# Optimization experiments

Measured on AMD Instinct MI355X. Metric: run time of the kernel, lower is better.

## Reference

```python
import jax, jax.numpy as jnp
import numpy as np

NB_TASKS = 20
CLASSES_PER_TASK = 100  # uniform cfg.increments -> cache_repeat
TOPK = 2
TEMPERATURE = 5.0  # cfg.task_temperature


def setup_inputs() -> dict:
    key = jax.random.key(0)
    k1, k2, k3 = jax.random.split(key, 3)
    B = 8192
    N = NB_TASKS * CLASSES_PER_TASK
    return {
        "gol": jax.random.normal(k1, (B, NB_TASKS), dtype=jnp.float32),
        "gocls": jax.random.normal(k2, (B, N), dtype=jnp.float32),
        "do_logit": jax.random.normal(k3, (B, N), dtype=jnp.float32),
        "alpha": jnp.array([0.5], dtype=jnp.float32),
    }


def _masked(gol_use, do_logit):
    # mask_ = softmax(gol_use / T, dim=1).repeat_interleave(cache_repeat, dim=1)
    soft = jax.nn.softmax(gol_use / TEMPERATURE, axis=1)  # [B, T]
    # topk hard mask, scattered then repeated; hard*soft repeated == repeat(hard*soft)
    k = min(gol_use.shape[1], TOPK)
    _, tk = jax.lax.top_k(gol_use, k)  # [B, k] int indices
    B = gol_use.shape[0]
    hard = jnp.zeros_like(gol_use).at[jnp.arange(B)[:, None], tk].set(1.0)
    mask = jnp.repeat(hard * soft, CLASSES_PER_TASK, axis=1)  # [B, N]
    return do_logit * mask


def reference(gol, gocls, do_logit, alpha):
    B = gol.shape[0]
    # gocl = opt_by_task(gate_cls_logit, increments, 'amax'): per-task max over class logits
    gocl = gocls.reshape(B, NB_TASKS, CLASSES_PER_TASK).max(axis=-1)  # [B, T]
    logit_mcm = _masked(gol, do_logit)
    logit_gcl = _masked(gocl, do_logit)
    lamb = alpha  # broadcasts over [B, N]
    logit_mix = lamb * logit_mcm + (1.0 - lamb) * logit_gcl
    return logit_mix
```

## Files before the change

kernel.cpp:

```cpp
#include <hip/hip_runtime.h>
#include <hip/hip_bf16.h>
#include <math.h>

#define NB_TASKS 20
#define CLASSES_PER_TASK 100
#define N_COLS (NB_TASKS * CLASSES_PER_TASK)
#define N_F4   (N_COLS / 4)
#define F4_PER_TASK (CLASSES_PER_TASK / 4)
#define INV_TEMP (1.0f / 5.0f)
#define ROWS_PER_BLOCK 4

__device__ __forceinline__ float rfl_f(float x) {
    return __int_as_float(__builtin_amdgcn_readfirstlane(__float_as_int(x)));
}

struct Top2 { int j1, j2; float w1, w2; };

__device__ __forceinline__ Top2 softmax_top2(float v, float coef, int lane) {
    float v1 = v; int i1 = lane;
    #pragma unroll
    for (int off = 16; off; off >>= 1) {
        float ov = __shfl_xor(v1, off);
        int   oj = __shfl_xor(i1, off);
        if (ov > v1 || (ov == v1 && oj < i1)) { v1 = ov; i1 = oj; }
    }
    float v2 = (lane == i1) ? -INFINITY : v;
    int   i2 = lane;
    #pragma unroll
    for (int off = 16; off; off >>= 1) {
        float ov = __shfl_xor(v2, off);
        int   oj = __shfl_xor(i2, off);
        if (ov > v2 || (ov == v2 && oj < i2)) { v2 = ov; i2 = oj; }
    }
    float ex  = __expf((v - v1) * INV_TEMP);
    float sum = ex;
    #pragma unroll
    for (int off = 16; off; off >>= 1)
        sum += __shfl_xor(sum, off);

    Top2 r;
    r.j1 = __builtin_amdgcn_readfirstlane(i1);
    r.j2 = __builtin_amdgcn_readfirstlane(i2);
    float w1 = coef / sum;
    float w2 = __expf((v2 - v1) * INV_TEMP) * w1;
    r.w1 = rfl_f(w1);
    r.w2 = rfl_f(w2);
    return r;
}

__global__ __launch_bounds__(256) void mix_kernel(
    const float* __restrict__ gol,
    const float* __restrict__ gocls,
    const float* __restrict__ dol,
    const float* __restrict__ alpha_p,
    float* __restrict__ out,
    int B)
{
    const int tid  = threadIdx.x;
    const int lane = tid & 63;
    const int b    = blockIdx.x * ROWS_PER_BLOCK + (tid >> 6);
    if (b >= B) return;

    const int grp = lane >> 4;
    const int s   = lane & 15;

    const float4* din  = (const float4*)(dol + (size_t)b * N_COLS);
    float4*       dout = (float4*)(out + (size_t)b * N_COLS);
    const float*  grow = gocls + (size_t)b * N_COLS;

    const float a  = alpha_p[0];
    const float gv = (lane < NB_TASKS) ? gol[(size_t)b * NB_TASKS + lane] : -INFINITY;

    {
        const float4 z = {0.0f, 0.0f, 0.0f, 0.0f};
        #pragma unroll
        for (int i = 0; i < (N_F4 + 63) / 64; ++i) {
            const int f = lane + 64 * i;
            if (f < N_F4) dout[f] = z;
        }
    }

    float cv = -INFINITY;
    #pragma unroll
    for (int k = 0; k < 5; ++k) {
        const float4* p = (const float4*)(grow + (4 * k + grp) * CLASSES_PER_TASK);
        float4 v0 = p[s];
        float m = fmaxf(fmaxf(v0.x, v0.y), fmaxf(v0.z, v0.w));
        if (s < 25 - 16) {
            float4 v1 = p[16 + s];
            m = fmaxf(m, fmaxf(fmaxf(v1.x, v1.y), fmaxf(v1.z, v1.w)));
        }
        #pragma unroll
        for (int off = 8; off; off >>= 1)
            m = fmaxf(m, __shfl_xor(m, off));
        float g2 = __shfl(m, (lane & 3) << 4);
        if ((lane >> 2) == k) cv = g2;
    }

    const Top2 pa = softmax_top2(gv, a,        lane);
    const Top2 pb = softmax_top2(cv, 1.0f - a, lane);

    asm volatile("s_waitcnt vmcnt(0)" ::: "memory");

    int   js[4] = {pa.j1, pa.j2, pb.j1, pb.j2};
    float ws[4] = {pa.w1, pa.w2, pb.w1, pb.w2};

    #pragma unroll
    for (int i = 0; i < 4; ++i) {
        bool first = true;
        #pragma unroll
        for (int k = 0; k < i; ++k) first = first && (js[k] != js[i]);
        if (first) {
            float w = ws[i];
            #pragma unroll
            for (int k = i + 1; k < 4; ++k) w += (js[k] == js[i]) ? ws[k] : 0.0f;
            if (lane < F4_PER_TASK) {
                const int f = js[i] * F4_PER_TASK + lane;
                float4 v = din[f];
                float4 r = {v.x * w, v.y * w, v.z * w, v.w * w};
                dout[f] = r;
            }
        }
    }
}

extern "C" void kernel_launch(void* const* d_in, const int* in_sizes, int n_in,
                              void* d_out, int out_size, void* d_ws, size_t ws_size,
                              hipStream_t stream) {
    const float* gol   = (const float*)d_in[0];
    const float* gocls = (const float*)d_in[1];
    const float* dol   = (const float*)d_in[2];
    const float* alpha = (const float*)d_in[3];
    float* out = (float*)d_out;

    const int B = in_sizes[0] / NB_TASKS;

    const int grid = (B + ROWS_PER_BLOCK - 1) / ROWS_PER_BLOCK;
    hipLaunchKernelGGL(mix_kernel, dim3(grid), dim3(256), 0, stream,
                       gol, gocls, dol, alpha, out, B);
}
```

Baseline: 28.31 us.

## Prefetch gol top-2 data early, skip redundant zero stores, use nontemporal stores

The gol-based top-2 is now computed before the zero-fill, so its two do_logit segments are loaded early and overlap the gocls max reduction. The zero-fill skips the gol top-2 task columns, which cuts the double write to those slots. All output writes use nontemporal stores. The code is restructured to avoid the 4-way dedup loop, and zero stores still overlap the later gocls-selected segments, which rely on the vmcnt wait for ordering.

```diff
diff --git a/kernel.cpp b/kernel.cpp
--- a/kernel.cpp
+++ b/kernel.cpp
@@ -9,6 +9,8 @@
 #define F4_PER_TASK (CLASSES_PER_TASK / 4)
 #define INV_TEMP (1.0f / 5.0f)
 #define ROWS_PER_BLOCK 4
+
+typedef float vf4 __attribute__((ext_vector_type(4)));
 
 __device__ __forceinline__ float rfl_f(float x) {
     return __int_as_float(__builtin_amdgcn_readfirstlane(__float_as_int(x)));
@@ -64,30 +66,41 @@
     const int grp = lane >> 4;
     const int s   = lane & 15;
 
-    const float4* din  = (const float4*)(dol + (size_t)b * N_COLS);
-    float4*       dout = (float4*)(out + (size_t)b * N_COLS);
-    const float*  grow = gocls + (size_t)b * N_COLS;
+    const vf4*   din  = (const vf4*)(dol + (size_t)b * N_COLS);
+    vf4*         dout = (vf4*)(out + (size_t)b * N_COLS);
+    const float* grow = gocls + (size_t)b * N_COLS;
 
     const float a  = alpha_p[0];
     const float gv = (lane < NB_TASKS) ? gol[(size_t)b * NB_TASKS + lane] : -INFINITY;
+    const Top2 pa = softmax_top2(gv, a, lane);
+
+    vf4 dA1 = {0,0,0,0}, dA2 = {0,0,0,0};
+    if (lane < F4_PER_TASK) {
+        dA1 = din[pa.j1 * F4_PER_TASK + lane];
+        dA2 = din[pa.j2 * F4_PER_TASK + lane];
+    }
 
     {
-        const float4 z = {0.0f, 0.0f, 0.0f, 0.0f};
+        const vf4 z = {0.0f, 0.0f, 0.0f, 0.0f};
         #pragma unroll
         for (int i = 0; i < (N_F4 + 63) / 64; ++i) {
             const int f = lane + 64 * i;
-            if (f < N_F4) dout[f] = z;
+            if (f < N_F4) {
+                const int task = f / F4_PER_TASK;
+                if (task != pa.j1 && task != pa.j2)
+                    __builtin_nontemporal_store(z, &dout[f]);
+            }
         }
     }
 
     float cv = -INFINITY;
     #pragma unroll
     for (int k = 0; k < 5; ++k) {
-        const float4* p = (const float4*)(grow + (4 * k + grp) * CLASSES_PER_TASK);
-        float4 v0 = p[s];
+        const vf4* p = (const vf4*)(grow + (4 * k + grp) * CLASSES_PER_TASK);
+        vf4 v0 = p[s];
         float m = fmaxf(fmaxf(v0.x, v0.y), fmaxf(v0.z, v0.w));
         if (s < 25 - 16) {
-            float4 v1 = p[16 + s];
+            vf4 v1 = p[16 + s];
             m = fmaxf(m, fmaxf(fmaxf(v1.x, v1.y), fmaxf(v1.z, v1.w)));
         }
         #pragma unroll
@@ -97,30 +110,29 @@
         if ((lane >> 2) == k) cv = g2;
     }
 
-    const Top2 pa = softmax_top2(gv, a,        lane);
     const Top2 pb = softmax_top2(cv, 1.0f - a, lane);
+
+    const float wA1 = pa.w1 + ((pb.j1 == pa.j1) ? pb.w1 : 0.0f)
+                            + ((pb.j2 == pa.j1) ? pb.w2 : 0.0f);
+    const float wA2 = pa.w2 + ((pb.j1 == pa.j2) ? pb.w1 : 0.0f)
+                            + ((pb.j2 == pa.j2) ? pb.w2 : 0.0f);
+    const bool bo1 = (pb.j1 != pa.j1) && (pb.j1 != pa.j2);
+    const bool bo2 = (pb.j2 != pa.j1) && (pb.j2 != pa.j2);
+
+    vf4 dB1 = {0,0,0,0}, dB2 = {0,0,0,0};
+    if (lane < F4_PER_TASK) {
+        if (bo1) dB1 = din[pb.j1 * F4_PER_TASK + lane];
+        if (bo2) dB2 = din[pb.j2 * F4_PER_TASK + lane];
+
+        __builtin_nontemporal_store(dA1 * wA1, &dout[pa.j1 * F4_PER_TASK + lane]);
+        __builtin_nontemporal_store(dA2 * wA2, &dout[pa.j2 * F4_PER_TASK + lane]);
+    }
 
     asm volatile("s_waitcnt vmcnt(0)" ::: "memory");
 
-    int   js[4] = {pa.j1, pa.j2, pb.j1, pb.j2};
-    float ws[4] = {pa.w1, pa.w2, pb.w1, pb.w2};
-
-    #pragma unroll
-    for (int i = 0; i < 4; ++i) {
-        bool first = true;
-        #pragma unroll
-        for (int k = 0; k < i; ++k) first = first && (js[k] != js[i]);
-        if (first) {
-            float w = ws[i];
-            #pragma unroll
-            for (int k = i + 1; k < 4; ++k) w += (js[k] == js[i]) ? ws[k] : 0.0f;
-            if (lane < F4_PER_TASK) {
-                const int f = js[i] * F4_PER_TASK + lane;
-                float4 v = din[f];
-                float4 r = {v.x * w, v.y * w, v.z * w, v.w * w};
-                dout[f] = r;
-            }
-        }
+    if (lane < F4_PER_TASK) {
+        if (bo1) __builtin_nontemporal_store(dB1 * pb.w1, &dout[pb.j1 * F4_PER_TASK + lane]);
+        if (bo2) __builtin_nontemporal_store(dB2 * pb.w2, &dout[pb.j2 * F4_PER_TASK + lane]);
     }
 }
 
```

After: 28.55 us. Within noise of the previous version (+0.8%).
